# Kernel optimization log

Measured on AMD Instinct MI355X. Metric: run time of the kernel, lower is better.

## Reference

```python
import jax, jax.numpy as jnp
import numpy as np
from functools import partial

PAD, SOD = 1, 2
VOCAB, E, H = 32000, 512, 512
BSZ, DOCLEN, SENTLEN, SRCLEN = 8, 16, 40, 400
MAXPOS = 62  # max_target_positions + 2
NEG = -1e9


def setup_inputs() -> dict:
    key = jax.random.key(0)
    ks = jax.random.split(key, 16)
    s = 0.05  # weight scale for numerical sanity
    emb = jax.random.normal(ks[0], (VOCAB, E), jnp.float32) * 0.1
    emb = emb.at[PAD].set(0.0)
    spe = jax.random.normal(ks[1], (MAXPOS, E), jnp.float32) * 0.1
    spe = spe.at[PAD].set(0.0)
    return {
        'prev_output_tokens': jax.random.randint(ks[2], (BSZ, DOCLEN, SENTLEN), 0, VOCAB),
        'encoder_out0': jax.random.normal(ks[3], (BSZ, SRCLEN, H), jnp.float32),
        'encoder_out1': jax.random.normal(ks[4], (BSZ, SRCLEN, H), jnp.float32),
        'encoder_padding_mask': jnp.zeros((BSZ, SRCLEN), bool),
        'embed_tokens': emb,
        'sent_pos_emb': spe,
        'w_ih_doc': jax.random.normal(ks[5], (4 * H, E), jnp.float32) * s,
        'w_hh_doc': jax.random.normal(ks[6], (4 * H, H), jnp.float32) * s,
        'b_ih_doc': jnp.zeros((4 * H,), jnp.float32),
        'b_hh_doc': jnp.zeros((4 * H,), jnp.float32),
        'attn_q_doc': jax.random.normal(ks[7], (H, H), jnp.float32) * s,
        'attn_o_doc': jax.random.normal(ks[8], (H, 2 * H), jnp.float32) * s,
        'w_ih_w': jax.random.normal(ks[9], (4 * H, E), jnp.float32) * s,
        'w_hh_w': jax.random.normal(ks[10], (4 * H, H), jnp.float32) * s,
        'b_ih_w': jnp.zeros((4 * H,), jnp.float32),
        'b_hh_w': jnp.zeros((4 * H,), jnp.float32),
        'attn_q_w': jax.random.normal(ks[11], (H, H), jnp.float32) * s,
        'attn_o_w': jax.random.normal(ks[12], (H, 2 * H), jnp.float32) * s,
        'fc_out_w': jax.random.normal(ks[13], (VOCAB, H), jnp.float32) * s,
        'fc_out_b': jnp.zeros((VOCAB,), jnp.float32),
    }


def _lstm_cell(x, h, c, w_ih, w_hh, b_ih, b_hh):
    g = x @ w_ih.T + h @ w_hh.T + b_ih + b_hh
    i, f, gg, o = jnp.split(g, 4, axis=-1)
    c = jax.nn.sigmoid(f) * c + jax.nn.sigmoid(i) * jnp.tanh(gg)
    h = jax.nn.sigmoid(o) * jnp.tanh(c)
    return h, c


def _attend(h, src, mask, wq, wo):
    # fairseq-style additive-bilinear attention: score = <src, Wq h>
    q = h @ wq.T                                  # [b, d]
    s = jnp.einsum('bsd,bd->bs', src, q)          # [b, srclen]
    s = jnp.where(mask, NEG, s)
    p = jax.nn.softmax(s, axis=-1)
    ctx = jnp.einsum('bs,bsd->bd', p, src)
    out = jnp.tanh(jnp.concatenate([ctx, h], axis=-1) @ wo.T)
    return out, p


def reference(prev_output_tokens, encoder_out0, encoder_out1, encoder_padding_mask,
              embed_tokens, sent_pos_emb,
              w_ih_doc, w_hh_doc, b_ih_doc, b_hh_doc, attn_q_doc, attn_o_doc,
              w_ih_w, w_hh_w, b_ih_w, b_hh_w, attn_q_w, attn_o_w,
              fc_out_w, fc_out_b):
    bsz, doclen, sentlen = prev_output_tokens.shape
    srclen = encoder_out0.shape[1]

    # ---- document-level LSTM + attention loop (one step per sentence) ----
    h0 = encoder_out0.mean(axis=1)                 # src_summary_h0
    x0 = jnp.broadcast_to(embed_tokens[SOD], (bsz, E))

    def doc_step(carry, _):
        h, c, inp = carry
        h, c = _lstm_cell(inp, h, c, w_ih_doc, w_hh_doc, b_ih_doc, b_hh_doc)
        out, _p = _attend(h, encoder_out0, encoder_padding_mask, attn_q_doc, attn_o_doc)
        return (h, c, out), out

    (_, _, last_out), doc_outs = jax.lax.scan(doc_step, (h0, h0, x0), None, length=doclen)
    sent_states = doc_outs.transpose(1, 0, 2).reshape(bsz * doclen, H)

    # ---- sentence positions (make_sent_positions) ----
    nonempty = (prev_output_tokens != PAD).sum(axis=2) != 0     # [bsz, doclen]
    pos = jnp.where(nonempty, PAD + 1 + jnp.arange(doclen), 1)
    sp = sent_pos_emb[pos.reshape(bsz * doclen)]                # [B2, E]

    # ---- word-level decoder over flattened sentences ----
    B2 = bsz * doclen
    ys = prev_output_tokens.reshape(B2, sentlen)
    x_in = embed_tokens[ys] + sp[:, None, :]                    # [B2, S, E]
    enc_w = jnp.repeat(encoder_out1, doclen, axis=0)            # [B2, srclen, d]
    mask_w = jnp.repeat(encoder_padding_mask, doclen, axis=0)

    def word_step(carry, x_t):
        h, c = carry
        h, c = _lstm_cell(x_t, h, c, w_ih_w, w_hh_w, b_ih_w, b_hh_w)
        out, p = _attend(h, enc_w, mask_w, attn_q_w, attn_o_w)
        return (h, c), (out, p)

    (_, _), (w_outs, w_scores) = jax.lax.scan(
        word_step, (sent_states, sent_states), x_in.transpose(1, 0, 2))
    w_outs = w_outs.transpose(1, 0, 2)                          # [B2, S, H]
    word_atte_scores = w_scores.transpose(1, 0, 2)              # [B2, S, srclen]

    logits = jnp.einsum('bsh,vh->bsv', w_outs, fc_out_w) + fc_out_b
    dec_outs = logits.reshape(bsz, doclen * sentlen, VOCAB)

    attn_scores = jnp.zeros((bsz, doclen, srclen), dec_outs.dtype)  # zeros as in original
    return dec_outs, attn_scores, word_atte_scores, last_out
```

## Files before the change

kernel.cpp:

```cpp
#include <hip/hip_runtime.h>
#include <cstdint>

typedef unsigned short u16;
typedef unsigned int u32;
typedef __attribute__((ext_vector_type(8))) short bf16x8;
typedef __attribute__((ext_vector_type(8))) unsigned short u16x8;
typedef __attribute__((ext_vector_type(4))) float f32x4;

struct us4 { u16 a, b, c, d; };

__device__ __forceinline__ u16 f2bf(float f) {
    uint32_t u = __float_as_uint(f);
    uint32_t r = (u + 0x7FFFu + ((u >> 16) & 1u)) >> 16;
    return (u16)r;
}
__device__ __forceinline__ float bf2f(u16 h) { return __uint_as_float(((uint32_t)h) << 16); }
__device__ __forceinline__ float sigm(float x) { return 1.f / (1.f + expf(-x)); }
__device__ __forceinline__ float dot4(float4 a, float4 b) {
    return a.x * b.x + a.y * b.y + a.z * b.z + a.w * b.w;
}
__device__ __forceinline__ float wave_sum(float v) {
#pragma unroll
    for (int o = 32; o; o >>= 1) v += __shfl_down(v, o);
    return v;
}
__device__ __forceinline__ float wave_max(float v) {
#pragma unroll
    for (int o = 32; o; o >>= 1) v = fmaxf(v, __shfl_down(v, o));
    return v;
}

__device__ __forceinline__ void ast(u32* p, u32 v) {
    __hip_atomic_store(p, v, __ATOMIC_RELAXED, __HIP_MEMORY_SCOPE_AGENT);
}
__device__ __forceinline__ u32 ald(const u32* p) {
    return __hip_atomic_load(p, __ATOMIC_RELAXED, __HIP_MEMORY_SCOPE_AGENT);
}
__device__ __forceinline__ u32 packsplit(float v) {
    u16 h = f2bf(v);
    u16 l = f2bf(v - bf2f(h));
    return (u32)h | ((u32)l << 16);
}

template <int NBLK, int NSHARD>
__device__ __forceinline__ void sbar(int* base, int idx) {
    __syncthreads();
    if (threadIdx.x == 0) {
        asm volatile("s_waitcnt vmcnt(0)" ::: "memory");
        int* genp = base + (NSHARD + 1) * 32;
        int g = __hip_atomic_load(genp, __ATOMIC_RELAXED, __HIP_MEMORY_SCOPE_AGENT);
        constexpr int SSIZE = NBLK / NSHARD;
        int* sc = base + (idx % NSHARD) * 32;
        bool released = false;
        if (__hip_atomic_fetch_add(sc, 1, __ATOMIC_RELAXED, __HIP_MEMORY_SCOPE_AGENT) == SSIZE - 1) {
            __hip_atomic_store(sc, 0, __ATOMIC_RELAXED, __HIP_MEMORY_SCOPE_AGENT);
            int* rc = base + NSHARD * 32;
            if (__hip_atomic_fetch_add(rc, 1, __ATOMIC_RELAXED, __HIP_MEMORY_SCOPE_AGENT) == NSHARD - 1) {
                __hip_atomic_store(rc, 0, __ATOMIC_RELAXED, __HIP_MEMORY_SCOPE_AGENT);
                __hip_atomic_store(genp, g + 1, __ATOMIC_RELAXED, __HIP_MEMORY_SCOPE_AGENT);
                released = true;
            }
        }
        if (!released) {
            while (__hip_atomic_load(genp, __ATOMIC_RELAXED, __HIP_MEMORY_SCOPE_AGENT) == g)
                __builtin_amdgcn_s_sleep(1);
        }
    }
    __syncthreads();
    asm volatile("" ::: "memory");
}

template <bool SPLIT, int AMODE, int EPI, int XMAJ = 0>
__global__ __launch_bounds__(256) void gemm_bt(
    const u16* __restrict__ AH, const u16* __restrict__ AL, int lda, long strideA,
    const u16* __restrict__ BH, const u16* __restrict__ BL, int ldb, long strideB,
    float* __restrict__ C, u16* __restrict__ CH, u16* __restrict__ CL,
    int ldc, long strideC, const float* __restrict__ bias, int K)
{
    constexpr int TL = 40;
    constexpr int CHK = 128 * TL;
    __shared__ u16 sm[(SPLIT ? 4 : 2) * CHK];
    u16* sAH = sm;
    u16* sBH = sm + CHK;
    u16* sAL = SPLIT ? sm + 2 * CHK : sm;
    u16* sBL = SPLIT ? sm + 3 * CHK : sm;

    const int tid = threadIdx.x;
    const int lane = tid & 63, w = tid >> 6;
    const int wm = w >> 1, wn = w & 1;
    const int lane15 = lane & 15, q8 = (lane >> 4) << 3;
    const int n0 = (XMAJ ? blockIdx.y : blockIdx.x) * 128;
    const int m0 = (XMAJ ? blockIdx.x : blockIdx.y) * 128;
    const int z = blockIdx.z;

    const int r = tid >> 2, c8 = (tid & 3) * 8;

    long aoff[2], boff[2];
#pragma unroll
    for (int h2 = 0; h2 < 2; ++h2) {
        int row = r + (h2 << 6);
        if (AMODE == 0) {
            aoff[h2] = strideA * z + (long)(m0 + row) * lda + c8;
        } else {
            int m = m0 + row;
            int t = m % 40, dd = m / 40;
            aoff[h2] = ((long)(t + 1) * 128 + (z * 16 + dd)) * 512 + c8;
        }
        boff[h2] = strideB * z + (long)(n0 + row) * ldb + c8;
    }

    f32x4 acc[4][4] = {};

    for (int k0 = 0; k0 < K; k0 += 32) {
#pragma unroll
        for (int h2 = 0; h2 < 2; ++h2) {
            int row = r + (h2 << 6);
            int sidx = row * TL + c8;
            *(u16x8*)&sAH[sidx] = *(const u16x8*)&AH[aoff[h2] + k0];
            *(u16x8*)&sBH[sidx] = *(const u16x8*)&BH[boff[h2] + k0];
            if constexpr (SPLIT) {
                *(u16x8*)&sAL[sidx] = *(const u16x8*)&AL[aoff[h2] + k0];
                *(u16x8*)&sBL[sidx] = *(const u16x8*)&BL[boff[h2] + k0];
            }
        }
        __syncthreads();

        bf16x8 a[4], b[4], al[4], bl[4];
#pragma unroll
        for (int i = 0; i < 4; ++i) {
            a[i] = *(const bf16x8*)&sAH[(wm * 64 + i * 16 + lane15) * TL + q8];
            b[i] = *(const bf16x8*)&sBH[(wn * 64 + i * 16 + lane15) * TL + q8];
            if constexpr (SPLIT) {
                al[i] = *(const bf16x8*)&sAL[(wm * 64 + i * 16 + lane15) * TL + q8];
                bl[i] = *(const bf16x8*)&sBL[(wn * 64 + i * 16 + lane15) * TL + q8];
            }
        }
#pragma unroll
        for (int mt = 0; mt < 4; ++mt)
#pragma unroll
            for (int nt = 0; nt < 4; ++nt) {
                acc[mt][nt] = __builtin_amdgcn_mfma_f32_16x16x32_bf16(a[mt], b[nt], acc[mt][nt], 0, 0, 0);
                if constexpr (SPLIT) {
                    acc[mt][nt] = __builtin_amdgcn_mfma_f32_16x16x32_bf16(a[mt], bl[nt], acc[mt][nt], 0, 0, 0);
                    acc[mt][nt] = __builtin_amdgcn_mfma_f32_16x16x32_bf16(al[mt], b[nt], acc[mt][nt], 0, 0, 0);
                }
            }
        __syncthreads();
    }

#pragma unroll
    for (int mt = 0; mt < 4; ++mt)
#pragma unroll
        for (int nt = 0; nt < 4; ++nt)
#pragma unroll
            for (int i = 0; i < 4; ++i) {
                int row = m0 + wm * 64 + mt * 16 + ((lane >> 4) << 2) + i;
                int col = n0 + wn * 64 + nt * 16 + lane15;
                long off = strideC * z + (long)row * ldc + col;
                float v = acc[mt][nt][i];
                if constexpr (EPI == 0) {
                    C[off] = v;
                } else if constexpr (EPI == 1) {
                    C[off] = v + bias[col];
                } else if constexpr (EPI == 2) {
                    u16 h_ = f2bf(v);
                    CH[off] = h_;
                    CL[off] = f2bf(v - bf2f(h_));
                } else if constexpr (EPI == 3) {
                    CH[off] = f2bf(tanhf(v));
                } else {
                    CH[off] = f2bf(v);
                }
            }
}

#define GLOAD_LDS16(gsrc, ldst) \
    __builtin_amdgcn_global_load_lds((const __attribute__((address_space(1))) u32*)(gsrc), \
                                     (__attribute__((address_space(3))) u32*)(ldst), 16, 0, 0)

__global__ __launch_bounds__(256) void gemm_lds_bias(
    const u16* __restrict__ A, const u16* __restrict__ B,
    float* __restrict__ C, const float* __restrict__ bias, int ldc, int K)
{
    __shared__ u16 sA[128 * 32];
    __shared__ u16 sB[128 * 32];

    const int tid = threadIdx.x;
    const int lane = tid & 63, w = tid >> 6;
    const int wm = w >> 1, wn = w & 1;
    const int lane15 = lane & 15, q8 = (lane >> 4) << 3;
    const int m0 = blockIdx.x * 128;
    const int n0 = blockIdx.y * 128;

    const int srow = lane >> 2, schunk = (lane & 3) * 8;

    f32x4 acc[4][4] = {};

    for (int k0 = 0; k0 < K; k0 += 32) {
#pragma unroll
        for (int c = 0; c < 2; ++c) {
            int base_r = (w * 2 + c) * 16;
            const u16* ga = A + (long)(m0 + base_r + srow) * 512 + k0 + schunk;
            const u16* gb = B + (long)(n0 + base_r + srow) * 512 + k0 + schunk;
            GLOAD_LDS16(ga, &sA[base_r * 32]);
            GLOAD_LDS16(gb, &sB[base_r * 32]);
        }
        __syncthreads();

        bf16x8 a[4], b[4];
#pragma unroll
        for (int i = 0; i < 4; ++i) {
            a[i] = *(const bf16x8*)&sA[(wm * 64 + i * 16 + lane15) * 32 + q8];
            b[i] = *(const bf16x8*)&sB[(wn * 64 + i * 16 + lane15) * 32 + q8];
        }
#pragma unroll
        for (int mt = 0; mt < 4; ++mt)
#pragma unroll
            for (int nt = 0; nt < 4; ++nt)
                acc[mt][nt] = __builtin_amdgcn_mfma_f32_16x16x32_bf16(a[mt], b[nt], acc[mt][nt], 0, 0, 0);
        __syncthreads();
    }

#pragma unroll
    for (int mt = 0; mt < 4; ++mt)
#pragma unroll
        for (int nt = 0; nt < 4; ++nt)
#pragma unroll
            for (int i = 0; i < 4; ++i) {
                int row = m0 + wm * 64 + mt * 16 + ((lane >> 4) << 2) + i;
                int col = n0 + wn * 64 + nt * 16 + lane15;
                C[(long)row * ldc + col] = acc[mt][nt][i] + bias[col];
            }
}

__global__ __launch_bounds__(256) void doc_mega(
    const float* __restrict__ enc0, const float* __restrict__ E0q,
    const float* __restrict__ E0o, const unsigned char* __restrict__ mask,
    const float* __restrict__ emb,
    const u16* __restrict__ WpH, const u16* __restrict__ WpL,
    const float* __restrict__ biasd, const float* __restrict__ wo_d,
    u32* __restrict__ dxP, u32* __restrict__ hP0, u32* __restrict__ hP1,
    u32* __restrict__ dcP, u32* __restrict__ dscP,
    float* __restrict__ dsent, float* __restrict__ out_last, int* bar)
{
    __shared__ u16 xhH[16 * 1032];
    __shared__ u16 xhL[16 * 1032];
    __shared__ float red4[4][16 * 17];
    __shared__ float aux2[512];
    __shared__ float sc_s[512];
    __shared__ float whoh_s[32];
    __shared__ float ctxp[8][32];
    __shared__ float rtmp[8];

    const int blk = blockIdx.x, tid = threadIdx.x;
    const int w = tid >> 6, lane = tid & 63;
    const int b_ = blk >> 4, s = blk & 15;
    const int lane15 = lane & 15, q8 = (lane >> 4) << 3;
    int* gbar = bar + 512 + b_ * 192;

    for (int q = tid; q < 8 * 1032; q += 256) { xhH[8 * 1032 + q] = 0; xhL[8 * 1032 + q] = 0; }

    {
        int dd = tid & 31, part = tid >> 5;
        const float* p0 = enc0 + ((long)b_ * 400 + part * 50) * 512 + s * 32 + dd;
        float sm = 0.f;
#pragma unroll 10
        for (int j = 0; j < 50; ++j) { sm += *p0; p0 += 512; }
        ctxp[part][dd] = sm;
        __syncthreads();
        if (tid < 32) {
            float m = 0.f;
#pragma unroll
            for (int p = 0; p < 8; ++p) m += ctxp[p][tid];
            m *= (1.f / 400.f);
            int e = s * 32 + tid;
            ast(&hP0[b_ * 512 + e], packsplit(m));
            ast(&dcP[b_ * 512 + e], __float_as_uint(m));
            ast(&dxP[b_ * 512 + e], packsplit(emb[1024 + e]));
        }
    }
    sbar<128, 8>(bar, blk);

    const int eb_b = tid & 7, eb_u4 = tid >> 3, eb_u = blk * 4 + eb_u4;
    float dcr = 0.f;
    if (tid < 32) dcr = __uint_as_float(ald(&dcP[eb_b * 512 + eb_u]));

    const u16* bh_base = WpH + ((long)blk * 16 + lane15) * 1024 + (w << 8) + q8;
    const u16* bl_base = WpL + ((long)blk * 16 + lane15) * 1024 + (w << 8) + q8;
    const u16* ah_base = xhH + lane15 * 1032 + (w << 8) + q8;
    const u16* al_base = xhL + lane15 * 1032 + (w << 8) + q8;

    for (int t = 0; t < 16; ++t) {
        u32* hinP = (t & 1) ? hP1 : hP0;
        u32* houtP = (t & 1) ? hP0 : hP1;

#pragma unroll
        for (int half = 0; half < 2; ++half) {
            u32 px[8], ph[8];
#pragma unroll
            for (int j = 0; j < 8; ++j) {
                int q = half * 2048 + j * 256 + tid;
                px[j] = ald(&dxP[q]);
                ph[j] = ald(&hinP[q]);
            }
#pragma unroll
            for (int j = 0; j < 8; ++j) {
                int q = half * 2048 + j * 256 + tid;
                int o = (q >> 9) * 1032 + (q & 511);
                xhH[o] = (u16)px[j];           xhL[o] = (u16)(px[j] >> 16);
                xhH[o + 512] = (u16)ph[j];     xhL[o + 512] = (u16)(ph[j] >> 16);
            }
        }
        __syncthreads();

        f32x4 acc = {};
#pragma unroll
        for (int k0 = 0; k0 < 256; k0 += 32) {
            bf16x8 aH = *(const bf16x8*)&ah_base[k0];
            bf16x8 aL = *(const bf16x8*)&al_base[k0];
            bf16x8 bH = *(const bf16x8*)&bh_base[k0];
            bf16x8 bL = *(const bf16x8*)&bl_base[k0];
            acc = __builtin_amdgcn_mfma_f32_16x16x32_bf16(aH, bH, acc, 0, 0, 0);
            acc = __builtin_amdgcn_mfma_f32_16x16x32_bf16(aH, bL, acc, 0, 0, 0);
            acc = __builtin_amdgcn_mfma_f32_16x16x32_bf16(aL, bH, acc, 0, 0, 0);
        }
#pragma unroll
        for (int i = 0; i < 4; ++i)
            red4[w][((lane >> 4) * 4 + i) * 17 + lane15] = acc[i];
        __syncthreads();

        if (tid < 32) {
            float g4[4];
#pragma unroll
            for (int g = 0; g < 4; ++g)
                g4[g] = red4[0][eb_b * 17 + eb_u4 * 4 + g] + red4[1][eb_b * 17 + eb_u4 * 4 + g]
                      + red4[2][eb_b * 17 + eb_u4 * 4 + g] + red4[3][eb_b * 17 + eb_u4 * 4 + g];
            float gi = g4[0] + biasd[eb_u];
            float gf = g4[1] + biasd[512 + eb_u];
            float gg = g4[2] + biasd[1024 + eb_u];
            float go = g4[3] + biasd[1536 + eb_u];
            dcr = sigm(gf) * dcr + sigm(gi) * tanhf(gg);
            float hv = sigm(go) * tanhf(dcr);
            ast(&houtP[eb_b * 512 + eb_u], packsplit(hv));
        }
        sbar<128, 8>(bar, blk);

        {
            u32 p0 = ald(&houtP[b_ * 512 + tid]);
            u32 p1 = ald(&houtP[b_ * 512 + 256 + tid]);
            aux2[tid] = bf2f((u16)p0) + bf2f((u16)(p0 >> 16));
            aux2[256 + tid] = bf2f((u16)p1) + bf2f((u16)(p1 >> 16));
            __syncthreads();
            for (int jj = w; jj < 25; jj += 4) {
                int j = s * 25 + jj;
                const float4* er = (const float4*)(E0q + ((long)b_ * 400 + j) * 512) + lane * 2;
                const float4* hv = (const float4*)aux2 + lane * 2;
                float sv = dot4(er[0], hv[0]) + dot4(er[1], hv[1]);
                sv = wave_sum(sv);
                if (lane == 0)
                    ast(&dscP[b_ * 400 + j], __float_as_uint(mask[b_ * 400 + j] ? -1e9f : sv));
            }
#pragma unroll
            for (int r = 0; r < 8; ++r) {
                int d = s * 32 + w * 8 + r;
                const float4* wr = (const float4*)(wo_d + (long)d * 1024 + 512) + lane * 2;
                const float4* hv = (const float4*)aux2 + lane * 2;
                float sv = dot4(wr[0], hv[0]) + dot4(wr[1], hv[1]);
                sv = wave_sum(sv);
                if (lane == 0) whoh_s[w * 8 + r] = sv;
            }
        }
        sbar<16, 4>(gbar, s);

        {
            float v0 = __uint_as_float(ald(&dscP[b_ * 400 + tid]));
            bool h1 = (tid + 256) < 400;
            float v1 = h1 ? __uint_as_float(ald(&dscP[b_ * 400 + tid + 256])) : -1e30f;
            float mx = wave_max(fmaxf(v0, v1));
            if (lane == 0) rtmp[w] = mx;
            __syncthreads();
            float M = fmaxf(fmaxf(rtmp[0], rtmp[1]), fmaxf(rtmp[2], rtmp[3]));
            float e0 = expf(v0 - M);
            float e1 = h1 ? expf(v1 - M) : 0.f;
            float sv = wave_sum(e0 + e1);
            if (lane == 0) rtmp[4 + w] = sv;
            __syncthreads();
            float inv = 1.f / (rtmp[4] + rtmp[5] + rtmp[6] + rtmp[7]);
            sc_s[tid] = e0 * inv;
            if (h1) sc_s[tid + 256] = e1 * inv;
            __syncthreads();
            int dd = tid & 31, part = tid >> 5;
            const float* eo = E0o + ((long)b_ * 400 + part * 50) * 512 + s * 32 + dd;
            float acc2 = 0.f;
#pragma unroll 10
            for (int j = 0; j < 50; ++j) { acc2 += sc_s[part * 50 + j] * (*eo); eo += 512; }
            ctxp[part][dd] = acc2;
            __syncthreads();
            if (tid < 32) {
                int d = s * 32 + tid;
                float o = whoh_s[tid];
#pragma unroll
                for (int p = 0; p < 8; ++p) o += ctxp[p][tid];
                float val = tanhf(o);
                ast(&dxP[b_ * 512 + d], packsplit(val));
                dsent[((b_ << 4) + t) * 512 + d] = val;
                if (t == 15) out_last[b_ * 512 + d] = val;
            }
        }
        sbar<128, 8>(bar, blk);
    }
}

__global__ __launch_bounds__(512) void word_mega(
    const float* __restrict__ sentS,
    u32* __restrict__ hAllP,
    u16* __restrict__ hAllH, u16* __restrict__ hAllL,
    const u16* __restrict__ WhhH, const u16* __restrict__ WhhL,
    const float* __restrict__ xW,
    u16* __restrict__ catB, int* bar)
{
    __shared__ float red[8][4][256];
    const int tid = threadIdx.x, blk = blockIdx.x;
    const int b2t = blk >> 5;
    const int u0 = (blk & 31) << 4;
    int* gbar = bar + 2048 + b2t * 192;

    float wcr = 0.f;
    long cidx = 0;
    int my_b2 = 0, my_u = 0;
    if (tid < 256) {
        my_b2 = b2t * 16 + (tid >> 4);
        my_u = u0 + (tid & 15);
        cidx = (long)my_b2 * 512 + my_u;
        wcr = sentS[cidx];
        ast(&hAllP[cidx], packsplit(wcr));
    }
    sbar<32, 4>(gbar, blk & 31);

    const int w = tid >> 6, lane = tid & 63;
    const int lane15 = lane & 15, q8 = (lane >> 4) << 3;
    const long arowE = (long)(b2t * 16 + lane15) * 512 + w * 64 + q8;
    long brow[4];
#pragma unroll
    for (int g = 0; g < 4; ++g)
        brow[g] = (long)(g * 512 + u0 + lane15) * 512 + w * 64 + q8;

    for (int t = 0; t < 40; ++t) {
        const u32* hP = hAllP + (long)t * 65536;

        u32 ph[16];
#pragma unroll
        for (int j = 0; j < 16; ++j)
            ph[j] = ald(&hP[arowE + (j >> 3) * 32 + (j & 7)]);

        float xw0 = 0.f, xw1 = 0.f, xw2 = 0.f, xw3 = 0.f;
        if (tid < 256) {
            const float* xr = xW + (long)t * 262144 + (long)my_b2 * 2048;
            xw0 = xr[my_u]; xw1 = xr[512 + my_u]; xw2 = xr[1024 + my_u]; xw3 = xr[1536 + my_u];
        }

        f32x4 acc[4] = {};
#pragma unroll
        for (int half = 0; half < 2; ++half) {
            int k0 = half * 32;
            bf16x8 aH, aL;
#pragma unroll
            for (int j = 0; j < 8; ++j) {
                u32 p = ph[half * 8 + j];
                aH[j] = (short)(p & 0xffffu);
                aL[j] = (short)(p >> 16);
            }
#pragma unroll
            for (int g = 0; g < 4; ++g) {
                bf16x8 bH = *(const bf16x8*)&WhhH[brow[g] + k0];
                bf16x8 bL = *(const bf16x8*)&WhhL[brow[g] + k0];
                acc[g] = __builtin_amdgcn_mfma_f32_16x16x32_bf16(aH, bH, acc[g], 0, 0, 0);
                acc[g] = __builtin_amdgcn_mfma_f32_16x16x32_bf16(aH, bL, acc[g], 0, 0, 0);
                acc[g] = __builtin_amdgcn_mfma_f32_16x16x32_bf16(aL, bH, acc[g], 0, 0, 0);
            }
        }
#pragma unroll
        for (int g = 0; g < 4; ++g)
#pragma unroll
            for (int i = 0; i < 4; ++i)
                red[w][g][((lane >> 4) * 4 + i) * 16 + lane15] = acc[g][i];
        __syncthreads();

        if (tid < 256) {
            float g4[4] = {0.f, 0.f, 0.f, 0.f};
#pragma unroll
            for (int ks = 0; ks < 8; ++ks)
#pragma unroll
                for (int g = 0; g < 4; ++g)
                    g4[g] += red[ks][g][tid];
            float gi = g4[0] + xw0;
            float gf = g4[1] + xw1;
            float gg = g4[2] + xw2;
            float go = g4[3] + xw3;
            wcr = sigm(gf) * wcr + sigm(gi) * tanhf(gg);
            float hv = sigm(go) * tanhf(wcr);
            u16 hh = f2bf(hv);
            u16 ll = f2bf(hv - bf2f(hh));
            long o = (long)(t + 1) * 65536 + cidx;
            ast(&hAllP[o], (u32)hh | ((u32)ll << 16));
            hAllH[o] = hh;
            hAllL[o] = ll;
            catB[((long)my_b2 * 40 + t) * 1024 + 512 + my_u] = hh;
        }
        sbar<32, 4>(gbar, blk & 31);
    }
}

__device__ __forceinline__ void split1(const float* __restrict__ src,
                                       u16* __restrict__ H, u16* __restrict__ L, long i)
{
    float4 v = ((const float4*)src)[i];
    u16 h0 = f2bf(v.x), h1 = f2bf(v.y), h2 = f2bf(v.z), h3 = f2bf(v.w);
    ((us4*)H)[i] = {h0, h1, h2, h3};
    ((us4*)L)[i] = {f2bf(v.x - bf2f(h0)), f2bf(v.y - bf2f(h1)),
                    f2bf(v.z - bf2f(h2)), f2bf(v.w - bf2f(h3))};
}
__device__ __forceinline__ void wqT1(const float* __restrict__ wq,
                                     u16* __restrict__ H, u16* __restrict__ L, int idx)
{
    int e = idx >> 9, d = idx & 511;
    float v = wq[(long)d * 512 + e];
    u16 h = f2bf(v);
    H[idx] = h;
    L[idx] = f2bf(v - bf2f(h));
}

__global__ __launch_bounds__(256) void prep_all(
    const float* __restrict__ wih_w, const float* __restrict__ whh_w,
    const float* __restrict__ enc1, const float* __restrict__ enc0,
    const float* __restrict__ wq_w, const float* __restrict__ wq_d,
    const float* __restrict__ wo_w, const float* __restrict__ fcw,
    const int* __restrict__ toks, const float* __restrict__ emb,
    const float* __restrict__ spe,
    const float* __restrict__ bih_w, const float* __restrict__ bhh_w,
    const float* __restrict__ bih_d, const float* __restrict__ bhh_d,
    const float* __restrict__ wih_d, const float* __restrict__ whh_d,
    const float* __restrict__ wo_d,
    u16* __restrict__ WihH, u16* __restrict__ WihL,
    u16* __restrict__ WhhH, u16* __restrict__ WhhL,
    u16* __restrict__ enc1H, u16* __restrict__ enc1L,
    u16* __restrict__ enc0H, u16* __restrict__ enc0L,
    u16* __restrict__ wqTH, u16* __restrict__ wqTL,
    u16* __restrict__ wqdTH, u16* __restrict__ wqdTL,
    u16* __restrict__ woB, u16* __restrict__ fcwB, u16* __restrict__ enc1T,
    u16* __restrict__ xinH, u16* __restrict__ xinL,
    u16* __restrict__ woCH, u16* __restrict__ woCL,
    u16* __restrict__ WpH, u16* __restrict__ WpL,
    float* __restrict__ biasc, float* __restrict__ biasd,
    float* __restrict__ out_attn, int* __restrict__ bar)
{
    int b = blockIdx.x;
    const int tid = threadIdx.x;

    if (b < 1024) { split1(wih_w, WihH, WihL, (long)b * 256 + tid); return; }
    b -= 1024;
    if (b < 1024) { split1(whh_w, WhhH, WhhL, (long)b * 256 + tid); return; }
    b -= 1024;
    if (b < 1600) { split1(enc1, enc1H, enc1L, (long)b * 256 + tid); return; }
    b -= 1600;
    if (b < 1600) { split1(enc0, enc0H, enc0L, (long)b * 256 + tid); return; }
    b -= 1600;
    if (b < 1024) { wqT1(wq_w, wqTH, wqTL, b * 256 + tid); return; }
    b -= 1024;
    if (b < 1024) { wqT1(wq_d, wqdTH, wqdTL, b * 256 + tid); return; }
    b -= 1024;
    if (b < 512) {
        long i = (long)b * 256 + tid;
        float4 v = ((const float4*)wo_w)[i];
        ((us4*)woB)[i] = {f2bf(v.x), f2bf(v.y), f2bf(v.z), f2bf(v.w)};
        return;
    }
    b -= 512;
    if (b < 16000) {
        long i = (long)b * 256 + tid;
        float4 v = ((const float4*)fcw)[i];
        ((us4*)fcwB)[i] = {f2bf(v.x), f2bf(v.y), f2bf(v.z), f2bf(v.w)};
        return;
    }
    b -= 16000;
    if (b < 6656) {
        long idx = (long)b * 256 + tid;
        int j = (int)(idx % 416);
        long be = idx / 416;
        int e = (int)(be % 512);
        int bb = (int)(be / 512);
        float v = (j < 400) ? enc1[((long)bb * 400 + j) * 512 + e] : 0.f;
        enc1T[idx] = f2bf(v);
        return;
    }
    b -= 6656;
    if (b < 1280) {
        int g = b * 256 + tid;
        int m = g >> 6, e0 = (g & 63) << 3;
        int t = m >> 7, b2 = m & 127;
        int ne = 0;
        for (int s = 0; s < 40; ++s) ne |= (toks[b2 * 40 + s] != 1);
        int pos = ne ? (2 + (b2 & 15)) : 1;
        const float* ep = emb + (long)toks[b2 * 40 + t] * 512 + e0;
        const float* sp = spe + (long)pos * 512 + e0;
        long o = (long)m * 512 + e0;
#pragma unroll
        for (int j = 0; j < 8; ++j) {
            float v = ep[j] + sp[j];
            u16 h = f2bf(v);
            xinH[o + j] = h;
            xinL[o + j] = f2bf(v - bf2f(h));
        }
        return;
    }
    b -= 1280;
    if (b < 1) {
        for (int i = tid; i < 2048; i += 256) {
            biasc[i] = bih_w[i] + bhh_w[i];
            biasd[i] = bih_d[i] + bhh_d[i];
        }
        return;
    }
    b -= 1;
    if (b < 200) {
        out_attn[b * 256 + tid] = 0.f;
        return;
    }
    b -= 200;
    if (b < 1024) {
        int i = b * 256 + tid;
        int d = i >> 9, e = i & 511;
        float v = wo_d[(long)d * 1024 + e];
        u16 h = f2bf(v);
        woCH[i] = h;
        woCL[i] = f2bf(v - bf2f(h));
        return;
    }
    b -= 1024;
    if (b < 1024) {
        long gidx = (long)b * 256 + tid;
        int r = (int)(gidx >> 7);
        int k8 = ((int)gidx & 127) * 8;
        int u = r >> 2, g = r & 3;
        long orow = (long)(g * 512 + u);
#pragma unroll
        for (int j = 0; j < 8; ++j) {
            int k = k8 + j;
            float v = (k < 512) ? wih_d[orow * 512 + k] : whh_d[orow * 512 + k - 512];
            u16 h = f2bf(v);
            WpH[(long)r * 1024 + k] = h;
            WpL[(long)r * 1024 + k] = f2bf(v - bf2f(h));
        }
        return;
    }
    b -= 1024;
    bar[b * 256 + tid] = 0;
}

__global__ __launch_bounds__(256) void word_softmax(
    const float* __restrict__ sc, const unsigned char* __restrict__ mask,
    float* __restrict__ pout, u16* __restrict__ pbf)
{
    const int r = blockIdx.x, tid = threadIdx.x;
    const int b = r / 640;
    const int wv = tid >> 6, lane = tid & 63;
    __shared__ float red[4];
    const int j1 = tid + 256;
    float v0 = sc[(long)r * 512 + tid];
    if (mask[b * 400 + tid]) v0 = -1e9f;
    float v1 = -1e30f;
    if (j1 < 400) {
        v1 = sc[(long)r * 512 + j1];
        if (mask[b * 400 + j1]) v1 = -1e9f;
    }
    float mv = wave_max(fmaxf(v0, v1));
    if (lane == 0) red[wv] = mv;
    __syncthreads();
    if (tid == 0) red[0] = fmaxf(fmaxf(red[0], red[1]), fmaxf(red[2], red[3]));
    __syncthreads();
    const float M = red[0];
    float e0 = expf(v0 - M);
    float e1 = (j1 < 400) ? expf(v1 - M) : 0.f;
    __syncthreads();
    float sv = wave_sum(e0 + e1);
    if (lane == 0) red[wv] = sv;
    __syncthreads();
    if (tid == 0) red[0] = red[0] + red[1] + red[2] + red[3];
    __syncthreads();
    const float inv = 1.f / red[0];
    float p0 = e0 * inv;
    pout[(long)r * 400 + tid] = p0;
    pbf[(long)r * 416 + tid] = f2bf(p0);
    if (j1 < 400) {
        float p1 = e1 * inv;
        pout[(long)r * 400 + j1] = p1;
        pbf[(long)r * 416 + j1] = f2bf(p1);
    } else if (j1 < 416) {
        pbf[(long)r * 416 + j1] = 0;
    }
}

extern "C" void kernel_launch(void* const* d_in, const int* in_sizes, int n_in,
                              void* d_out, int out_size, void* d_ws, size_t ws_size,
                              hipStream_t stream)
{
    (void)in_sizes; (void)n_in; (void)out_size; (void)ws_size;

    const int*   toks  = (const int*)  d_in[0];
    const float* enc0  = (const float*)d_in[1];
    const float* enc1  = (const float*)d_in[2];
    const unsigned char* mask = (const unsigned char*)d_in[3];
    const float* emb   = (const float*)d_in[4];
    const float* spe   = (const float*)d_in[5];
    const float* wih_d = (const float*)d_in[6];
    const float* whh_d = (const float*)d_in[7];
    const float* bih_d = (const float*)d_in[8];
    const float* bhh_d = (const float*)d_in[9];
    const float* wq_d  = (const float*)d_in[10];
    const float* wo_d  = (const float*)d_in[11];
    const float* wih_w = (const float*)d_in[12];
    const float* whh_w = (const float*)d_in[13];
    const float* bih_w = (const float*)d_in[14];
    const float* bhh_w = (const float*)d_in[15];
    const float* wq_w  = (const float*)d_in[16];
    const float* wo_w  = (const float*)d_in[17];
    const float* fcw   = (const float*)d_in[18];
    const float* fcb   = (const float*)d_in[19];

    float* out_dec  = (float*)d_out;
    float* out_attn = out_dec + 163840000L;
    float* out_watt = out_attn + 51200;
    float* out_last = out_watt + 2048000;

    char* wsp = (char*)d_ws;
    auto alloc = [&](size_t bytes) -> void* {
        void* p = wsp;
        wsp += (bytes + 255) & ~(size_t)255;
        return p;
    };

    float* xW    = (float*)alloc(40L * 128 * 2048 * 4);
    u32* hAllP   = (u32*)alloc(41L * 128 * 512 * 4);
    u16* hAllH   = (u16*)alloc(41L * 128 * 512 * 2);
    u16* hAllL   = (u16*)alloc(41L * 128 * 512 * 2);
    u16* xinH    = (u16*)alloc(5120L * 512 * 2);
    u16* xinL    = (u16*)alloc(5120L * 512 * 2);
    u16* WihH    = (u16*)alloc(2048L * 512 * 2);
    u16* WihL    = (u16*)alloc(2048L * 512 * 2);
    u16* WhhH    = (u16*)alloc(2048L * 512 * 2);
    u16* WhhL    = (u16*)alloc(2048L * 512 * 2);
    u16* wqTH    = (u16*)alloc(512L * 512 * 2);
    u16* wqTL    = (u16*)alloc(512L * 512 * 2);
    u16* wqdTH   = (u16*)alloc(512L * 512 * 2);
    u16* wqdTL   = (u16*)alloc(512L * 512 * 2);
    u16* enc1H   = (u16*)alloc(3200L * 512 * 2);
    u16* enc1L   = (u16*)alloc(3200L * 512 * 2);
    u16* enc0H   = (u16*)alloc(3200L * 512 * 2);
    u16* enc0L   = (u16*)alloc(3200L * 512 * 2);
    u16* sq1H    = (u16*)alloc(3328L * 512 * 2);
    u16* sq1L    = (u16*)alloc(3328L * 512 * 2);
    float* E0q   = (float*)alloc(3200L * 512 * 4);
    float* E0o   = (float*)alloc(3200L * 512 * 4);
    u16* woCH    = (u16*)alloc(512L * 512 * 2);
    u16* woCL    = (u16*)alloc(512L * 512 * 2);
    u16* WpH     = (u16*)alloc(2048L * 1024 * 2);
    u16* WpL     = (u16*)alloc(2048L * 1024 * 2);
    float* wsS   = (float*)alloc(5120L * 512 * 4);
    u16* Pbf     = (u16*)alloc(5120L * 416 * 2);
    u16* enc1T   = (u16*)alloc(8L * 512 * 416 * 2);
    u16* catB    = (u16*)alloc(5120L * 1024 * 2);
    u16* woB     = (u16*)alloc(512L * 1024 * 2);
    u16* Alog    = (u16*)alloc(5120L * 512 * 2);
    u16* fcwB    = (u16*)alloc(32000L * 512 * 2);
    float* biasc = (float*)alloc(2048 * 4);
    float* biasd = (float*)alloc(2048 * 4);
    u32* dxP     = (u32*)alloc(4096 * 4);
    u32* hP0     = (u32*)alloc(4096 * 4);
    u32* hP1     = (u32*)alloc(4096 * 4);
    u32* dcP     = (u32*)alloc(4096 * 4);
    u32* dscP    = (u32*)alloc(3200 * 4);
    float* dsent = (float*)alloc(128L * 512 * 4);
    int* bar     = (int*)alloc(4096 * 4);

    prep_all<<<dim3(34009), 256, 0, stream>>>(
        wih_w, whh_w, enc1, enc0, wq_w, wq_d, wo_w, fcw, toks, emb, spe,
        bih_w, bhh_w, bih_d, bhh_d, wih_d, whh_d, wo_d,
        WihH, WihL, WhhH, WhhL, enc1H, enc1L, enc0H, enc0L,
        wqTH, wqTL, wqdTH, wqdTL, woB, fcwB, enc1T, xinH, xinL,
        woCH, woCL, WpH, WpL, biasc, biasd, out_attn, bar);

    gemm_bt<true, 0, 2><<<dim3(4, 25, 1), 256, 0, stream>>>(
        enc1H, enc1L, 512, 0, wqTH, wqTL, 512, 0,
        nullptr, sq1H, sq1L, 512, 0, nullptr, 512);

    gemm_bt<true, 0, 0><<<dim3(4, 25, 1), 256, 0, stream>>>(
        enc0H, enc0L, 512, 0, wqdTH, wqdTL, 512, 0,
        E0q, nullptr, nullptr, 512, 0, nullptr, 512);

    gemm_bt<true, 0, 0><<<dim3(4, 25, 1), 256, 0, stream>>>(
        enc0H, enc0L, 512, 0, woCH, woCL, 512, 0,
        E0o, nullptr, nullptr, 512, 0, nullptr, 512);

    gemm_bt<true, 0, 1><<<dim3(16, 40, 1), 256, 0, stream>>>(
        xinH, xinL, 512, 0, WihH, WihL, 512, 0,
        xW, nullptr, nullptr, 2048, 0, biasc, 512);

    doc_mega<<<dim3(128), 256, 0, stream>>>(
        enc0, E0q, E0o, mask, emb, WpH, WpL, biasd, wo_d,
        dxP, hP0, hP1, dcP, dscP, dsent, out_last, bar);

    word_mega<<<dim3(256), 512, 0, stream>>>(
        dsent, hAllP, hAllH, hAllL, WhhH, WhhL, xW, catB, bar);

    gemm_bt<true, 1, 0><<<dim3(4, 5, 8), 256, 0, stream>>>(
        hAllH, hAllL, 0, 0, sq1H, sq1L, 512, 204800L,
        wsS, nullptr, nullptr, 512, 327680L, nullptr, 512);

    word_softmax<<<dim3(5120), 256, 0, stream>>>(wsS, mask, out_watt, Pbf);

    gemm_bt<false, 0, 4><<<dim3(4, 5, 8), 256, 0, stream>>>(
        Pbf, nullptr, 416, 266240L, enc1T, nullptr, 416, 212992L,
        nullptr, catB, nullptr, 1024, 655360L, nullptr, 416);

    gemm_bt<false, 0, 3><<<dim3(4, 40, 1), 256, 0, stream>>>(
        catB, nullptr, 1024, 0, woB, nullptr, 1024, 0,
        nullptr, Alog, nullptr, 512, 0, nullptr, 1024);

    gemm_lds_bias<<<dim3(40, 250, 1), 256, 0, stream>>>(
        Alog, fcwB, out_dec, fcb, 32000, 512);
}
```

Before: 1.111 ms.

## Replace sharded counter barrier with flag barrier and fuse head GEMMs

Replaces the sharded atomic-counter grid barrier with a per-block flag barrier: each block stores a monotonically increasing generation and lanes poll every peer's flag. The aim is to cut barrier latency in the sequential doc and word recurrence kernels. The four independent head GEMMs are merged into one launch of 940 blocks to save launch overhead and fill more CUs. The final logits store becomes nontemporal. Costs are more polling traffic per barrier and a larger flag buffer, which prep_all must clear.

```diff
diff --git a/kernel.cpp b/kernel.cpp
--- a/kernel.cpp
+++ b/kernel.cpp
@@ -42,29 +42,14 @@
     return (u32)h | ((u32)l << 16);
 }
 
-template <int NBLK, int NSHARD>
-__device__ __forceinline__ void sbar(int* base, int idx) {
+template <int NBLK>
+__device__ __forceinline__ void fbar(u32* flags, int me, u32 gen) {
+    asm volatile("s_waitcnt vmcnt(0)" ::: "memory");
     __syncthreads();
-    if (threadIdx.x == 0) {
-        asm volatile("s_waitcnt vmcnt(0)" ::: "memory");
-        int* genp = base + (NSHARD + 1) * 32;
-        int g = __hip_atomic_load(genp, __ATOMIC_RELAXED, __HIP_MEMORY_SCOPE_AGENT);
-        constexpr int SSIZE = NBLK / NSHARD;
-        int* sc = base + (idx % NSHARD) * 32;
-        bool released = false;
-        if (__hip_atomic_fetch_add(sc, 1, __ATOMIC_RELAXED, __HIP_MEMORY_SCOPE_AGENT) == SSIZE - 1) {
-            __hip_atomic_store(sc, 0, __ATOMIC_RELAXED, __HIP_MEMORY_SCOPE_AGENT);
-            int* rc = base + NSHARD * 32;
-            if (__hip_atomic_fetch_add(rc, 1, __ATOMIC_RELAXED, __HIP_MEMORY_SCOPE_AGENT) == NSHARD - 1) {
-                __hip_atomic_store(rc, 0, __ATOMIC_RELAXED, __HIP_MEMORY_SCOPE_AGENT);
-                __hip_atomic_store(genp, g + 1, __ATOMIC_RELAXED, __HIP_MEMORY_SCOPE_AGENT);
-                released = true;
-            }
-        }
-        if (!released) {
-            while (__hip_atomic_load(genp, __ATOMIC_RELAXED, __HIP_MEMORY_SCOPE_AGENT) == g)
-                __builtin_amdgcn_s_sleep(1);
-        }
+    if (threadIdx.x == 0) ast(&flags[me * 32], gen);
+    if (threadIdx.x < NBLK) {
+        while (ald(&flags[threadIdx.x * 32]) < gen)
+            __builtin_amdgcn_s_sleep(1);
     }
     __syncthreads();
     asm volatile("" ::: "memory");
@@ -174,6 +159,112 @@
             }
 }
 
+__global__ __launch_bounds__(256) void gemm_head(
+    const u16* __restrict__ enc1H, const u16* __restrict__ enc1L,
+    const u16* __restrict__ wqTH,  const u16* __restrict__ wqTL,
+    const u16* __restrict__ enc0H, const u16* __restrict__ enc0L,
+    const u16* __restrict__ wqdTH, const u16* __restrict__ wqdTL,
+    const u16* __restrict__ woCH,  const u16* __restrict__ woCL,
+    const u16* __restrict__ xinH,  const u16* __restrict__ xinL,
+    const u16* __restrict__ WihH,  const u16* __restrict__ WihL,
+    u16* __restrict__ sq1H, u16* __restrict__ sq1L,
+    float* __restrict__ E0q, float* __restrict__ E0o,
+    float* __restrict__ xW, const float* __restrict__ biasc)
+{
+    constexpr int TL = 40;
+    constexpr int CHK = 128 * TL;
+    __shared__ u16 sm[4 * CHK];
+    u16* sAH = sm;
+    u16* sBH = sm + CHK;
+    u16* sAL = sm + 2 * CHK;
+    u16* sBL = sm + 3 * CHK;
+
+    const int bid = blockIdx.x;
+    const u16 *AH, *AL, *BH, *BL;
+    int task, n0, m0, ldc;
+    if (bid < 300) {
+        task = bid / 100;
+        int rr = bid % 100;
+        n0 = (rr & 3) * 128; m0 = (rr >> 2) * 128; ldc = 512;
+        if (task == 0)      { AH = enc1H; AL = enc1L; BH = wqTH;  BL = wqTL;  }
+        else if (task == 1) { AH = enc0H; AL = enc0L; BH = wqdTH; BL = wqdTL; }
+        else                { AH = enc0H; AL = enc0L; BH = woCH;  BL = woCL;  }
+    } else {
+        task = 3;
+        int rr = bid - 300;
+        n0 = (rr & 15) * 128; m0 = (rr >> 4) * 128; ldc = 2048;
+        AH = xinH; AL = xinL; BH = WihH; BL = WihL;
+    }
+
+    const int tid = threadIdx.x;
+    const int lane = tid & 63, w = tid >> 6;
+    const int wm = w >> 1, wn = w & 1;
+    const int lane15 = lane & 15, q8 = (lane >> 4) << 3;
+    const int r = tid >> 2, c8 = (tid & 3) * 8;
+
+    long aoff[2], boff[2];
+#pragma unroll
+    for (int h2 = 0; h2 < 2; ++h2) {
+        int row = r + (h2 << 6);
+        aoff[h2] = (long)(m0 + row) * 512 + c8;
+        boff[h2] = (long)(n0 + row) * 512 + c8;
+    }
+
+    f32x4 acc[4][4] = {};
+    for (int k0 = 0; k0 < 512; k0 += 32) {
+#pragma unroll
+        for (int h2 = 0; h2 < 2; ++h2) {
+            int row = r + (h2 << 6);
+            int sidx = row * TL + c8;
+            *(u16x8*)&sAH[sidx] = *(const u16x8*)&AH[aoff[h2] + k0];
+            *(u16x8*)&sBH[sidx] = *(const u16x8*)&BH[boff[h2] + k0];
+            *(u16x8*)&sAL[sidx] = *(const u16x8*)&AL[aoff[h2] + k0];
+            *(u16x8*)&sBL[sidx] = *(const u16x8*)&BL[boff[h2] + k0];
+        }
+        __syncthreads();
+        bf16x8 a[4], b[4], al[4], bl[4];
+#pragma unroll
+        for (int i = 0; i < 4; ++i) {
+            a[i]  = *(const bf16x8*)&sAH[(wm * 64 + i * 16 + lane15) * TL + q8];
+            b[i]  = *(const bf16x8*)&sBH[(wn * 64 + i * 16 + lane15) * TL + q8];
+            al[i] = *(const bf16x8*)&sAL[(wm * 64 + i * 16 + lane15) * TL + q8];
+            bl[i] = *(const bf16x8*)&sBL[(wn * 64 + i * 16 + lane15) * TL + q8];
+        }
+#pragma unroll
+        for (int mt = 0; mt < 4; ++mt)
+#pragma unroll
+            for (int nt = 0; nt < 4; ++nt) {
+                acc[mt][nt] = __builtin_amdgcn_mfma_f32_16x16x32_bf16(a[mt],  b[nt],  acc[mt][nt], 0, 0, 0);
+                acc[mt][nt] = __builtin_amdgcn_mfma_f32_16x16x32_bf16(a[mt],  bl[nt], acc[mt][nt], 0, 0, 0);
+                acc[mt][nt] = __builtin_amdgcn_mfma_f32_16x16x32_bf16(al[mt], b[nt],  acc[mt][nt], 0, 0, 0);
+            }
+        __syncthreads();
+    }
+
+#pragma unroll
+    for (int mt = 0; mt < 4; ++mt)
+#pragma unroll
+        for (int nt = 0; nt < 4; ++nt)
+#pragma unroll
+            for (int i = 0; i < 4; ++i) {
+                int row = m0 + wm * 64 + mt * 16 + ((lane >> 4) << 2) + i;
+                int col = n0 + wn * 64 + nt * 16 + lane15;
+                long off = (long)row * ldc + col;
+                float v = acc[mt][nt][i];
+                if (task == 0) {
+                    u16 h_ = f2bf(v);
+                    sq1H[off] = h_;
+                    sq1L[off] = f2bf(v - bf2f(h_));
+                } else if (task == 1) {
+                    E0q[off] = v;
+                } else if (task == 2) {
+                    E0o[off] = v;
+                } else {
+                    xW[off] = v + biasc[col];
+                }
+            }
+}
+
 #define GLOAD_LDS16(gsrc, ldst) \
     __builtin_amdgcn_global_load_lds((const __attribute__((address_space(1))) u32*)(gsrc), \
                                      (__attribute__((address_space(3))) u32*)(ldst), 16, 0, 0)
@@ -229,7 +320,7 @@
             for (int i = 0; i < 4; ++i) {
                 int row = m0 + wm * 64 + mt * 16 + ((lane >> 4) << 2) + i;
                 int col = n0 + wn * 64 + nt * 16 + lane15;
-                C[(long)row * ldc + col] = acc[mt][nt][i] + bias[col];
+                __builtin_nontemporal_store(acc[mt][nt][i] + bias[col], &C[(long)row * ldc + col]);
             }
 }
 
@@ -241,7 +332,7 @@
     const float* __restrict__ biasd, const float* __restrict__ wo_d,
     u32* __restrict__ dxP, u32* __restrict__ hP0, u32* __restrict__ hP1,
     u32* __restrict__ dcP, u32* __restrict__ dscP,
-    float* __restrict__ dsent, float* __restrict__ out_last, int* bar)
+    float* __restrict__ dsent, float* __restrict__ out_last, u32* bar)
 {
     __shared__ u16 xhH[16 * 1032];
     __shared__ u16 xhL[16 * 1032];
@@ -256,7 +347,9 @@
     const int w = tid >> 6, lane = tid & 63;
     const int b_ = blk >> 4, s = blk & 15;
     const int lane15 = lane & 15, q8 = (lane >> 4) << 3;
-    int* gbar = bar + 512 + b_ * 192;
+    u32* fF = bar;
+    u32* fG = bar + 4096 + b_ * 512;
+    u32 genF = 0, genG = 0;
 
     for (int q = tid; q < 8 * 1032; q += 256) { xhH[8 * 1032 + q] = 0; xhL[8 * 1032 + q] = 0; }
 
@@ -279,7 +372,7 @@
             ast(&dxP[b_ * 512 + e], packsplit(emb[1024 + e]));
         }
     }
-    sbar<128, 8>(bar, blk);
+    fbar<128>(fF, blk, ++genF);
 
     const int eb_b = tid & 7, eb_u4 = tid >> 3, eb_u = blk * 4 + eb_u4;
     float dcr = 0.f;
@@ -343,7 +436,7 @@
             float hv = sigm(go) * tanhf(dcr);
             ast(&houtP[eb_b * 512 + eb_u], packsplit(hv));
         }
-        sbar<128, 8>(bar, blk);
+        fbar<128>(fF, blk, ++genF);
 
         {
             u32 p0 = ald(&houtP[b_ * 512 + tid]);
@@ -370,7 +463,7 @@
                 if (lane == 0) whoh_s[w * 8 + r] = sv;
             }
         }
-        sbar<16, 4>(gbar, s);
+        fbar<16>(fG, s, ++genG);
 
         {
             float v0 = __uint_as_float(ald(&dscP[b_ * 400 + tid]));
@@ -407,7 +500,7 @@
                 if (t == 15) out_last[b_ * 512 + d] = val;
             }
         }
-        sbar<128, 8>(bar, blk);
+        fbar<128>(fF, blk, ++genF);
     }
 }
 
@@ -417,13 +510,14 @@
     u16* __restrict__ hAllH, u16* __restrict__ hAllL,
     const u16* __restrict__ WhhH, const u16* __restrict__ WhhL,
     const float* __restrict__ xW,
-    u16* __restrict__ catB, int* bar)
+    u16* __restrict__ catB, u32* bar)
 {
     __shared__ float red[8][4][256];
     const int tid = threadIdx.x, blk = blockIdx.x;
     const int b2t = blk >> 5;
     const int u0 = (blk & 31) << 4;
-    int* gbar = bar + 2048 + b2t * 192;
+    u32* fG = bar + 8192 + b2t * 1024;
+    u32 genG = 0;
 
     float wcr = 0.f;
     long cidx = 0;
@@ -435,7 +529,7 @@
         wcr = sentS[cidx];
         ast(&hAllP[cidx], packsplit(wcr));
     }
-    sbar<32, 4>(gbar, blk & 31);
+    fbar<32>(fG, blk & 31, ++genG);
 
     const int w = tid >> 6, lane = tid & 63;
     const int lane15 = lane & 15, q8 = (lane >> 4) << 3;
@@ -507,7 +601,7 @@
             hAllL[o] = ll;
             catB[((long)my_b2 * 40 + t) * 1024 + 512 + my_u] = hh;
         }
-        sbar<32, 4>(gbar, blk & 31);
+        fbar<32>(fG, blk & 31, ++genG);
     }
 }
 
@@ -552,7 +646,7 @@
     u16* __restrict__ woCH, u16* __restrict__ woCL,
     u16* __restrict__ WpH, u16* __restrict__ WpL,
     float* __restrict__ biasc, float* __restrict__ biasd,
-    float* __restrict__ out_attn, int* __restrict__ bar)
+    float* __restrict__ out_attn, u32* __restrict__ bar)
 {
     int b = blockIdx.x;
     const int tid = threadIdx.x;
@@ -780,30 +874,19 @@
     u32* dcP     = (u32*)alloc(4096 * 4);
     u32* dscP    = (u32*)alloc(3200 * 4);
     float* dsent = (float*)alloc(128L * 512 * 4);
-    int* bar     = (int*)alloc(4096 * 4);
-
-    prep_all<<<dim3(34009), 256, 0, stream>>>(
+    u32* bar     = (u32*)alloc(16384 * 4);
+
+    prep_all<<<dim3(34057), 256, 0, stream>>>(
         wih_w, whh_w, enc1, enc0, wq_w, wq_d, wo_w, fcw, toks, emb, spe,
         bih_w, bhh_w, bih_d, bhh_d, wih_d, whh_d, wo_d,
         WihH, WihL, WhhH, WhhL, enc1H, enc1L, enc0H, enc0L,
         wqTH, wqTL, wqdTH, wqdTL, woB, fcwB, enc1T, xinH, xinL,
         woCH, woCL, WpH, WpL, biasc, biasd, out_attn, bar);
 
-    gemm_bt<true, 0, 2><<<dim3(4, 25, 1), 256, 0, stream>>>(
-        enc1H, enc1L, 512, 0, wqTH, wqTL, 512, 0,
-        nullptr, sq1H, sq1L, 512, 0, nullptr, 512);
-
-    gemm_bt<true, 0, 0><<<dim3(4, 25, 1), 256, 0, stream>>>(
-        enc0H, enc0L, 512, 0, wqdTH, wqdTL, 512, 0,
-        E0q, nullptr, nullptr, 512, 0, nullptr, 512);
-
-    gemm_bt<true, 0, 0><<<dim3(4, 25, 1), 256, 0, stream>>>(
-        enc0H, enc0L, 512, 0, woCH, woCL, 512, 0,
-        E0o, nullptr, nullptr, 512, 0, nullptr, 512);
-
-    gemm_bt<true, 0, 1><<<dim3(16, 40, 1), 256, 0, stream>>>(
-        xinH, xinL, 512, 0, WihH, WihL, 512, 0,
-        xW, nullptr, nullptr, 2048, 0, biasc, 512);
+    gemm_head<<<dim3(940), 256, 0, stream>>>(
+        enc1H, enc1L, wqTH, wqTL, enc0H, enc0L, wqdTH, wqdTL,
+        woCH, woCL, xinH, xinL, WihH, WihL,
+        sq1H, sq1L, E0q, E0o, xW, biasc);
 
     doc_mega<<<dim3(128), 256, 0, stream>>>(
         enc0, E0q, E0o, mask, emb, WpH, WpL, biasd, wo_d,
```

Result: faster. 977.1 us (-12.1%).
